# Kernel optimization log

Hardware: AMD Instinct MI355X
Metric: run time of the kernel (lower is better)

The kernel has to match this reference:

```python
import jax, jax.numpy as jnp
import numpy as np

ALPHA = 0.2  # LeakyReLU negative slope
NEG_INF = -9e15


def gat_layer(x, W, a, adj, concat):
    # x: [N, Fin], W: [Fin, Fout], a: [2*Fout, 1], adj: [N, N] (>0 = edge)
    h = x @ W                              # [N, Fout]
    Fout = W.shape[1]
    a_left = a[:Fout, 0]                   # scores from source (row) node
    a_right = a[Fout:, 0]                  # scores from target (col) node
    # e_ij = leakyrelu(a_left . h_i + a_right . h_j)  -- equivalent to the
    # concat-pairwise formulation without materializing [N, N, 2F]
    e = jax.nn.leaky_relu((h @ a_left)[:, None] + (h @ a_right)[None, :], ALPHA)
    e = jnp.where(adj > 0, e, NEG_INF)     # masked scores [N, N]
    att = jax.nn.softmax(e, axis=1)
    h_prime = att @ h                      # [N, Fout]
    return jax.nn.elu(h_prime) if concat else h_prime


def setup_inputs() -> dict:
    key = jax.random.key(0)
    ks = jax.random.split(key, 6)
    N, Din, Dh, Dout, H = 4096, 256, 64, 64, 8
    features = jax.random.normal(ks[0], (N, Din), dtype=jnp.float32)
    adj = jax.random.randint(ks[1], (N, N), 0, 2, dtype=jnp.int32)

    def xavier(k, shape, gain=1.414):
        fan_in, fan_out = shape[0], shape[1]
        bound = gain * np.sqrt(6.0 / (fan_in + fan_out))
        return jax.random.uniform(k, shape, jnp.float32, -bound, bound)

    W_h = jnp.stack([xavier(k, (Din, Dh)) for k in jax.random.split(ks[2], H)])        # [H, Din, Dh]
    a_h = jnp.stack([xavier(k, (2 * Dh, 1)) for k in jax.random.split(ks[3], H)])      # [H, 2Dh, 1]
    W_out = xavier(ks[4], (Dh * H, Dout))
    a_out = xavier(ks[5], (2 * Dout, 1))
    return {"features": features, "adj": adj, "W_h": W_h, "a_h": a_h,
            "W_out": W_out, "a_out": a_out}


def reference(features, adj, W_h, a_h, W_out, a_out):
    # eval mode: dropout layers are identity
    heads = jax.vmap(lambda W, a: gat_layer(features, W, a, adj, True))(W_h, a_h)  # [H, N, Dh]
    H, N, Dh = heads.shape
    x = jnp.transpose(heads, (1, 0, 2)).reshape(N, H * Dh)   # concat along feature dim
    return gat_layer(x, W_out, a_out, adj, False)            # [N, Dout]
```

## Files before the change

kernel.cpp:

```cpp
#include <hip/hip_runtime.h>
#include <hip/hip_fp16.h>

constexpr int NV  = 4096;
constexpr int DIN = 256;
constexpr int DH  = 64;
constexpr int NH  = 8;
constexpr int K2  = 512;
constexpr int Z2  = 8;

typedef _Float16 half8 __attribute__((ext_vector_type(8)));
typedef float f32x4 __attribute__((ext_vector_type(4)));
typedef unsigned u32x4 __attribute__((ext_vector_type(4)));

__device__ __forceinline__ unsigned fkey(float x) {
    unsigned b = __float_as_uint(x);
    return b ^ ((unsigned)((int)b >> 31) | 0x80000000u);
}
__device__ __forceinline__ float fkey_inv(unsigned key) {
    unsigned b = (key & 0x80000000u) ? (key ^ 0x80000000u) : ~key;
    return __uint_as_float(b);
}

__global__ void prep_kernel(const float* __restrict__ feat,
                            const float* __restrict__ Wh,
                            const float* __restrict__ ah,
                            const float* __restrict__ Wout,
                            const float* __restrict__ aout,
                            _Float16* __restrict__ xf16,
                            _Float16* __restrict__ WTh,
                            _Float16* __restrict__ WTo,
                            float* __restrict__ aLR,
                            unsigned* __restrict__ maxkey)
{
    int tid = blockIdx.x * blockDim.x + threadIdx.x;
    int nth = gridDim.x * blockDim.x;
    for (int i = tid; i < NV*DIN; i += nth) xf16[i] = (_Float16)feat[i];
    for (int i = tid; i < NH*DH*DIN; i += nth) {
        int h = i >> 14, n = (i >> 8) & 63, k = i & 255;
        WTh[i] = (_Float16)Wh[(h*DIN + k)*DH + n];
    }
    for (int i = tid; i < DH*K2; i += nth) {
        int n = i >> 9, k = i & 511;
        WTo[i] = (_Float16)Wout[k*DH + n];
    }
    for (int i = tid; i < NH*DH; i += nth) {
        int h = i >> 6, j = i & 63;
        aLR[i]          = ah[h*128 + j];
        aLR[NH*DH + i]  = ah[h*128 + 64 + j];
    }
    for (int i = tid; i < DH; i += nth) {
        aLR[2*NH*DH + i]      = aout[i];
        aLR[2*NH*DH + DH + i] = aout[64 + i];
    }
    if (tid < 16) maxkey[tid] = 0u;
}

__global__ void adjmask_kernel(const int* __restrict__ adj,
                               unsigned long long* __restrict__ mask)
{
    int row = blockIdx.x;
    int wave = threadIdx.x >> 6, lane = threadIdx.x & 63;
    for (int g = wave; g < 64; g += 4) {
        int v = adj[(size_t)row*NV + g*64 + lane];
        unsigned long long b = __ballot(v > 0);
        if (lane == 0) mask[(size_t)row*64 + g] = b;
    }
}

template<int K>
__global__ __launch_bounds__(256) void gemm_kernel(
    const _Float16* __restrict__ A,
    const _Float16* __restrict__ WT,
    const float* __restrict__ aL,
    const float* __restrict__ aR,
    _Float16* __restrict__ hT,
    float* __restrict__ hl,
    float* __restrict__ hr,
    unsigned* __restrict__ maxkey)
{
    const int head = blockIdx.y;
    const int i0 = blockIdx.x * 64;
    const int t = threadIdx.x;
    const int wave = t >> 6, lane = t & 63, m = lane & 15, q = lane >> 4;

    const _Float16* Ap = A + (size_t)(i0 + wave*16 + m) * K + q*8;
    const _Float16* Wp = WT + (size_t)head*DH*K + (size_t)m*K + q*8;

    f32x4 acc0 = {0.f,0.f,0.f,0.f}, acc1 = acc0, acc2 = acc0, acc3 = acc0;
    for (int k0 = 0; k0 < K; k0 += 32) {
        half8 a  = *(const half8*)(Ap + k0);
        half8 b0 = *(const half8*)(Wp + k0);
        half8 b1 = *(const half8*)(Wp + 16*K + k0);
        half8 b2 = *(const half8*)(Wp + 32*K + k0);
        half8 b3 = *(const half8*)(Wp + 48*K + k0);
        acc0 = __builtin_amdgcn_mfma_f32_16x16x32_f16(a, b0, acc0, 0, 0, 0);
        acc1 = __builtin_amdgcn_mfma_f32_16x16x32_f16(a, b1, acc1, 0, 0, 0);
        acc2 = __builtin_amdgcn_mfma_f32_16x16x32_f16(a, b2, acc2, 0, 0, 0);
        acc3 = __builtin_amdgcn_mfma_f32_16x16x32_f16(a, b3, acc3, 0, 0, 0);
    }

    __shared__ _Float16 T[64][80];
    const int rb = wave*16 + q*4;
    for (int r = 0; r < 4; r++) {
        T[ 0 + m][rb + r] = (_Float16)acc0[r];
        T[16 + m][rb + r] = (_Float16)acc1[r];
        T[32 + m][rb + r] = (_Float16)acc2[r];
        T[48 + m][rb + r] = (_Float16)acc3[r];
    }
    __syncthreads();

    {
        int d = t >> 2, seg = t & 3;
        half8* dst = (half8*)(hT + (size_t)(head*DH + d)*NV + i0 + seg*16);
        dst[0] = *(const half8*)&T[d][seg*16];
        dst[1] = *(const half8*)&T[d][seg*16 + 8];
    }
    __shared__ float red[2][4][64];
    {
        int il = t & 63, part = t >> 6;
        float sl = 0.f, sr = 0.f;
        for (int kk = 0; kk < 16; kk++) {
            int k = part*16 + kk;
            float hv = (float)T[k][il];
            sl += hv * aL[head*DH + k];
            sr += hv * aR[head*DH + k];
        }
        red[0][part][il] = sl;
        red[1][part][il] = sr;
    }
    __syncthreads();
    if (t < 64) {
        float sl = red[0][0][t] + red[0][1][t] + red[0][2][t] + red[0][3][t];
        float sr = red[1][0][t] + red[1][1][t] + red[1][2][t] + red[1][3][t];
        hl[head*NV + i0 + t] = sl;
        hr[head*NV + i0 + t] = sr;
        unsigned key = fkey(sr);
        for (int off = 32; off > 0; off >>= 1) {
            unsigned o = __shfl_xor(key, off);
            key = key > o ? key : o;
        }
        if (t == 0) atomicMax(maxkey + head, key);
    }
}

__global__ __launch_bounds__(256) void gemm2_kernel(
    const _Float16* __restrict__ A,
    const _Float16* __restrict__ WT,
    const float* __restrict__ aL,
    const float* __restrict__ aR,
    _Float16* __restrict__ hT,
    float* __restrict__ hl,
    float* __restrict__ hr,
    unsigned* __restrict__ maxkey)
{
    const int i0 = blockIdx.x * 16;
    const int t = threadIdx.x;
    const int w = t >> 6, lane = t & 63, m = lane & 15, q = lane >> 4;

    const _Float16* Ap = A + (size_t)(i0 + m)*K2 + w*128 + q*8;
    const _Float16* Wp = WT + (size_t)m*K2 + w*128 + q*8;

    f32x4 zero4 = {0.f,0.f,0.f,0.f};
    f32x4 acc[4] = {zero4, zero4, zero4, zero4};
    #pragma unroll
    for (int k0 = 0; k0 < 128; k0 += 32) {
        half8 a = *(const half8*)(Ap + k0);
        #pragma unroll
        for (int nt = 0; nt < 4; nt++) {
            half8 b = *(const half8*)(Wp + (size_t)nt*16*K2 + k0);
            acc[nt] = __builtin_amdgcn_mfma_f32_16x16x32_f16(a, b, acc[nt], 0, 0, 0);
        }
    }

    __shared__ float Cred[4][16][68];
    #pragma unroll
    for (int r = 0; r < 4; r++)
        #pragma unroll
        for (int nt = 0; nt < 4; nt++)
            Cred[w][q*4 + r][nt*16 + m] = acc[nt][r];
    __syncthreads();

    const int col = t & 63, r0 = (t >> 6) * 4;
    #pragma unroll
    for (int rr = 0; rr < 4; rr++) {
        int row = r0 + rr;
        float s = Cred[0][row][col] + Cred[1][row][col]
                + Cred[2][row][col] + Cred[3][row][col];
        hT[(size_t)col*NV + i0 + row] = (_Float16)s;
        Cred[0][row][col] = s;
    }
    __syncthreads();
    if (t < 16) {
        float sl = 0.f, sr = 0.f;
        for (int c = 0; c < 64; c++) {
            float v = Cred[0][t][c];
            sl += v * aL[c];
            sr += v * aR[c];
        }
        hl[i0 + t] = sl;
        hr[i0 + t] = sr;
        atomicMax(maxkey, fkey(sr));
    }
}

template<int MODE>
__global__ __launch_bounds__(256, 8) void att_kernel(
    const _Float16* __restrict__ hT,
    const float* __restrict__ hl,
    const float* __restrict__ hr,
    const unsigned* __restrict__ maxkey,
    const unsigned* __restrict__ adjm32,
    float* __restrict__ accz,
    float* __restrict__ lz)
{
    const int head = (MODE == 0) ? blockIdx.y : 0;
    const int i0 = blockIdx.x * 64;
    const int t = threadIdx.x;
    const int wave = t >> 6, lane = t & 63, m = lane & 15, q = lane >> 4;
    const int row = wave*16 + m;

    __shared__ _Float16 BT[64][136];
    __shared__ float hr1_s[128];
    __shared__ unsigned mask_s[64][4];
    __shared__ float a1_s[64], a2_s[64];

    const float L2E = 1.4426950408889634f;
    const float maxhr = fkey_inv(maxkey[head]);

    if (t < 64) {
        float v = hl[head*NV + i0 + t];
        float e = v + maxhr;
        float mi = fmaxf(e, 0.2f*e) * L2E;
        float a1 = v*L2E - mi;
        float a2 = 0.2f*L2E*v - mi;
        a1_s[t] = a1;
        a2_s[t] = a2 - 0.2f*a1;
    }

    f32x4 zero4 = {0.f,0.f,0.f,0.f};
    f32x4 acc[4] = {zero4, zero4, zero4, zero4};
    f32x4 accl = zero4;
    half8 ones;
    #pragma unroll
    for (int u = 0; u < 8; u++) ones[u] = (_Float16)1.0f;

    const int ntiles = 32 / gridDim.z;
    const int tile0  = blockIdx.z * ntiles;

    for (int tt = 0; tt < ntiles; tt++) {
        const int j0 = (tile0 + tt) * 128;
        #pragma unroll
        for (int ii = 0; ii < 4; ii++) {
            int d = (t >> 4) + ii*16;
            *(half8*)&BT[d][(t & 15)*8] =
                *(const half8*)(hT + (size_t)(head*DH + d)*NV + j0 + (t & 15)*8);
        }
        if (t < 128) hr1_s[t] = hr[head*NV + j0 + t] * L2E;
        mask_s[t >> 2][t & 3] = adjm32[(size_t)(i0 + (t >> 2))*128 + (j0 >> 5) + (t & 3)];
        __syncthreads();

        const float a1 = a1_s[row], a2p = a2_s[row];
        const u32x4 mkv = *(const u32x4*)&mask_s[row][0];
        #pragma unroll
        for (int ks = 0; ks < 4; ks++) {
            const int jj = ks*32 + q*8;
            const unsigned mk8 = mkv[ks] >> (q*8);
            f32x4 h0 = *(const f32x4*)&hr1_s[jj];
            f32x4 h1 = *(const f32x4*)&hr1_s[jj + 4];
            half8 a;
            #pragma unroll
            for (int u = 0; u < 8; u++) {
                float hv = (u < 4) ? h0[u] : h1[u - 4];
                float t1 = a1 + hv;
                float t2 = fmaf(0.2f, t1, a2p);
                float tm = fmaxf(t1, t2);
                tm = ((mk8 >> u) & 1u) ? tm : -10000.0f;
                a[u] = (_Float16)__builtin_amdgcn_exp2f(tm);
            }
            half8 b0 = *(const half8*)&BT[ 0 + m][jj];
            half8 b1 = *(const half8*)&BT[16 + m][jj];
            half8 b2 = *(const half8*)&BT[32 + m][jj];
            half8 b3 = *(const half8*)&BT[48 + m][jj];
            acc[0] = __builtin_amdgcn_mfma_f32_16x16x32_f16(a, b0, acc[0], 0, 0, 0);
            acc[1] = __builtin_amdgcn_mfma_f32_16x16x32_f16(a, b1, acc[1], 0, 0, 0);
            acc[2] = __builtin_amdgcn_mfma_f32_16x16x32_f16(a, b2, acc[2], 0, 0, 0);
            acc[3] = __builtin_amdgcn_mfma_f32_16x16x32_f16(a, b3, acc[3], 0, 0, 0);
            accl   = __builtin_amdgcn_mfma_f32_16x16x32_f16(a, ones, accl, 0, 0, 0);
        }
        __syncthreads();
    }

    #pragma unroll
    for (int r = 0; r < 4; r++) {
        const int orow = wave*16 + q*4 + r;
        const int i = i0 + orow;
        if (MODE == 0) {
            float* dst = accz + ((size_t)blockIdx.z*NV + i)*K2 + head*DH;
            #pragma unroll
            for (int nt = 0; nt < 4; nt++) dst[nt*16 + m] = acc[nt][r];
            if (m == 0) lz[((size_t)blockIdx.z*NH + head)*NV + i] = accl[r];
        } else {
            float* dst = accz + ((size_t)blockIdx.z*NV + i)*DH;
            #pragma unroll
            for (int nt = 0; nt < 4; nt++) dst[nt*16 + m] = acc[nt][r];
            if (m == 0) lz[(size_t)blockIdx.z*NV + i] = accl[r];
        }
    }
}

__global__ void combine_x2_kernel(const float* __restrict__ accz,
                                  const float* __restrict__ lz,
                                  _Float16* __restrict__ x2, int Z1)
{
    const float L2E = 1.4426950408889634f;
    int idx = blockIdx.x * blockDim.x + threadIdx.x;
    int i = idx >> 9, h = (idx & 511) >> 6;
    float s = 0.f, l = 0.f;
    for (int z = 0; z < Z1; z++) {
        s += accz[(size_t)z*NV*K2 + idx];
        l += lz[((size_t)z*NH + h)*NV + i];
    }
    float v = l > 0.f ? s / l : 0.f;
    v = v > 0.f ? v : (__builtin_amdgcn_exp2f(v * L2E) - 1.f);
    x2[idx] = (_Float16)v;
}

__global__ void finalize_kernel(const float* __restrict__ accz,
                                const float* __restrict__ lz,
                                float* __restrict__ out)
{
    int idx = blockIdx.x * blockDim.x + threadIdx.x;
    int i = idx >> 6;
    float s = 0.f, l = 0.f;
    #pragma unroll
    for (int z = 0; z < Z2; z++) {
        s += accz[(size_t)z*NV*DH + idx];
        l += lz[(size_t)z*NV + i];
    }
    out[idx] = l > 0.f ? s / l : 0.f;
}

extern "C" void kernel_launch(void* const* d_in, const int* in_sizes, int n_in,
                              void* d_out, int out_size, void* d_ws, size_t ws_size,
                              hipStream_t stream)
{
    const float* feat = (const float*)d_in[0];
    const int* adj    = (const int*)d_in[1];
    const float* Wh   = (const float*)d_in[2];
    const float* ah   = (const float*)d_in[3];
    const float* Wout = (const float*)d_in[4];
    const float* aout = (const float*)d_in[5];

    char* p = (char*)d_ws;
    auto alloc = [&](size_t bytes) { char* r = p; p += (bytes + 255) & ~255ull; return r; };

    _Float16* xf16 = (_Float16*)alloc((size_t)NV*DIN*2);
    _Float16* WTh  = (_Float16*)alloc((size_t)NH*DH*DIN*2);
    _Float16* WTo  = (_Float16*)alloc((size_t)DH*K2*2);
    float*    aLR  = (float*)alloc((2*NH*DH + 2*DH)*4);
    unsigned* maxkey = (unsigned*)alloc(16*4);
    unsigned long long* adjm = (unsigned long long*)alloc((size_t)NV*64*8);
    _Float16* hT1 = (_Float16*)alloc((size_t)NH*DH*NV*2);
    float* hl1 = (float*)alloc((size_t)NH*NV*4);
    float* hr1 = (float*)alloc((size_t)NH*NV*4);
    _Float16* x2  = (_Float16*)alloc((size_t)NV*K2*2);
    _Float16* hT2 = (_Float16*)alloc((size_t)DH*NV*2);
    float* acc2z = (float*)alloc((size_t)Z2*NV*DH*4);
    float* l2z   = (float*)alloc((size_t)Z2*NV*4);
    float* hl2 = (float*)alloc(NV*4);
    float* hr2 = (float*)alloc(NV*4);

    size_t used = (size_t)(p - (char*)d_ws);
    size_t per_z = (size_t)NV*K2*4 + (size_t)NH*NV*4 + 512;
    size_t avail = ws_size > used ? ws_size - used : 0;
    int Z1 = (avail >= 4*per_z + 4096) ? 4 : 2;
    float* acc1z = (float*)alloc((size_t)Z1*NV*K2*4);
    float* l1z   = (float*)alloc((size_t)Z1*NH*NV*4);

    prep_kernel<<<256, 256, 0, stream>>>(feat, Wh, ah, Wout, aout, xf16, WTh, WTo, aLR, maxkey);
    adjmask_kernel<<<NV, 256, 0, stream>>>(adj, adjm);
    gemm_kernel<DIN><<<dim3(64, NH), 256, 0, stream>>>(xf16, WTh, aLR, aLR + NH*DH,
                                                       hT1, hl1, hr1, maxkey);
    att_kernel<0><<<dim3(64, NH, Z1), 256, 0, stream>>>(hT1, hl1, hr1, maxkey,
                                                        (const unsigned*)adjm, acc1z, l1z);
    combine_x2_kernel<<<dim3(NV*K2/256), 256, 0, stream>>>(acc1z, l1z, x2, Z1);
    gemm2_kernel<<<dim3(NV/16), 256, 0, stream>>>(x2, WTo, aLR + 2*NH*DH, aLR + 2*NH*DH + DH,
                                                  hT2, hl2, hr2, maxkey + 8);
    att_kernel<1><<<dim3(64, 1, Z2), 256, 0, stream>>>(hT2, hl2, hr2, maxkey + 8,
                                                       (const unsigned*)adjm, acc2z, l2z);
    finalize_kernel<<<dim3(NV*DH/256), 256, 0, stream>>>(acc2z, l2z, (float*)d_out);
}
```

Baseline: 230.0 us.

## Factor attention exponentials into separable row/column terms and widen attention tiles

The per-element exp2 in the attention kernels is replaced by a factorization: exp(leakyrelu(l+r)) becomes the max of two products, exp(l)*exp(r) and exp(0.2l)*exp(0.2r). Each product is a precomputed fp16 row factor times a column factor, stabilised by a per-128-column tile max that the GEMM kernels now record with atomics. This removes per-element transcendental work, leaving a half-precision multiply, max and bitmask per element. Layer-one attention now processes two 16-row m-tiles per wave (128 rows per block) to reuse the loaded B tiles, with launch bounds relaxed to 4 blocks. The adjacency-bitmask kernel is merged into the prep kernel to save a launch. The risk is fp16 range and precision loss in the factored products. The kernel also now reads a single maxkey slot for every head, which only shifts a per-row constant.

```diff
diff --git a/kernel.cpp b/kernel.cpp
--- a/kernel.cpp
+++ b/kernel.cpp
@@ -21,7 +21,10 @@
     return __uint_as_float(b);
 }
 
+constexpr int NKEYS = 304;
+
 __global__ void prep_kernel(const float* __restrict__ feat,
+                            const int* __restrict__ adj,
                             const float* __restrict__ Wh,
                             const float* __restrict__ ah,
                             const float* __restrict__ Wout,
@@ -30,10 +33,21 @@
                             _Float16* __restrict__ WTh,
                             _Float16* __restrict__ WTo,
                             float* __restrict__ aLR,
-                            unsigned* __restrict__ maxkey)
-{
-    int tid = blockIdx.x * blockDim.x + threadIdx.x;
-    int nth = gridDim.x * blockDim.x;
+                            unsigned* __restrict__ keys,
+                            unsigned long long* __restrict__ mask)
+{
+    if (blockIdx.x < NV) {
+        int row = blockIdx.x;
+        int wave = threadIdx.x >> 6, lane = threadIdx.x & 63;
+        for (int g = wave; g < 64; g += 4) {
+            int v = adj[(size_t)row*NV + g*64 + lane];
+            unsigned long long b = __ballot(v > 0);
+            if (lane == 0) mask[(size_t)row*64 + g] = b;
+        }
+        return;
+    }
+    int tid = (blockIdx.x - NV) * blockDim.x + threadIdx.x;
+    int nth = 256 * 256;
     for (int i = tid; i < NV*DIN; i += nth) xf16[i] = (_Float16)feat[i];
     for (int i = tid; i < NH*DH*DIN; i += nth) {
         int h = i >> 14, n = (i >> 8) & 63, k = i & 255;
@@ -52,19 +66,7 @@
         aLR[2*NH*DH + i]      = aout[i];
         aLR[2*NH*DH + DH + i] = aout[64 + i];
     }
-    if (tid < 16) maxkey[tid] = 0u;
-}
-
-__global__ void adjmask_kernel(const int* __restrict__ adj,
-                               unsigned long long* __restrict__ mask)
-{
-    int row = blockIdx.x;
-    int wave = threadIdx.x >> 6, lane = threadIdx.x & 63;
-    for (int g = wave; g < 64; g += 4) {
-        int v = adj[(size_t)row*NV + g*64 + lane];
-        unsigned long long b = __ballot(v > 0);
-        if (lane == 0) mask[(size_t)row*64 + g] = b;
-    }
+    if (tid < NKEYS) keys[tid] = 0u;
 }
 
 template<int K>
@@ -76,7 +78,8 @@
     _Float16* __restrict__ hT,
     float* __restrict__ hl,
     float* __restrict__ hr,
-    unsigned* __restrict__ maxkey)
+    unsigned* __restrict__ maxkey,
+    unsigned* __restrict__ mtkey)
 {
     const int head = blockIdx.y;
     const int i0 = blockIdx.x * 64;
@@ -139,7 +142,10 @@
             unsigned o = __shfl_xor(key, off);
             key = key > o ? key : o;
         }
-        if (t == 0) atomicMax(maxkey + head, key);
+        if (t == 0) {
+            atomicMax(maxkey + head, key);
+            atomicMax(mtkey + head*32 + (i0 >> 7), key);
+        }
     }
 }
 
@@ -151,7 +157,8 @@
     _Float16* __restrict__ hT,
     float* __restrict__ hl,
     float* __restrict__ hr,
-    unsigned* __restrict__ maxkey)
+    unsigned* __restrict__ maxkey,
+    unsigned* __restrict__ mtkey)
 {
     const int i0 = blockIdx.x * 16;
     const int t = threadIdx.x;
@@ -199,47 +206,62 @@
         }
         hl[i0 + t] = sl;
         hr[i0 + t] = sr;
-        atomicMax(maxkey, fkey(sr));
-    }
-}
-
-template<int MODE>
-__global__ __launch_bounds__(256, 8) void att_kernel(
+        unsigned key = fkey(sr);
+        atomicMax(maxkey, key);
+        atomicMax(mtkey + (i0 >> 7), key);
+    }
+}
+
+template<int MODE, int NMT>
+__global__ __launch_bounds__(256, 4) void att_kernel(
     const _Float16* __restrict__ hT,
     const float* __restrict__ hl,
     const float* __restrict__ hr,
     const unsigned* __restrict__ maxkey,
+    const unsigned* __restrict__ mtkey,
     const unsigned* __restrict__ adjm32,
     float* __restrict__ accz,
     float* __restrict__ lz)
 {
     const int head = (MODE == 0) ? blockIdx.y : 0;
-    const int i0 = blockIdx.x * 64;
+    const int i0 = blockIdx.x * (NMT*64);
     const int t = threadIdx.x;
     const int wave = t >> 6, lane = t & 63, m = lane & 15, q = lane >> 4;
-    const int row = wave*16 + m;
 
     __shared__ _Float16 BT[64][136];
-    __shared__ float hr1_s[128];
-    __shared__ unsigned mask_s[64][4];
-    __shared__ float a1_s[64], a2_s[64];
+    __shared__ __align__(16) _Float16 Fs[128], Gs[128];
+    __shared__ __align__(16) unsigned mask_s[NMT*64][4];
+    __shared__ float b1_s[NMT*64], b2_s[NMT*64];
 
     const float L2E = 1.4426950408889634f;
-    const float maxhr = fkey_inv(maxkey[head]);
-
-    if (t < 64) {
+    const float maxhr = fkey_inv(*maxkey);
+
+    if (t < NMT*64) {
         float v = hl[head*NV + i0 + t];
-        float e = v + maxhr;
-        float mi = fmaxf(e, 0.2f*e) * L2E;
-        float a1 = v*L2E - mi;
-        float a2 = 0.2f*L2E*v - mi;
-        a1_s[t] = a1;
-        a2_s[t] = a2 - 0.2f*a1;
+        float X = v + maxhr;
+        float mm = fmaxf(X, 0.2f*X) * L2E;
+        b1_s[t] = __builtin_amdgcn_exp2f(v*L2E - mm);
+        b2_s[t] = __builtin_amdgcn_exp2f(0.2f*L2E*v - mm);
+    }
+    __syncthreads();
+
+    float b1r[NMT], b2r[NMT];
+    #pragma unroll
+    for (int mt = 0; mt < NMT; mt++) {
+        int row = wave*(NMT*16) + mt*16 + m;
+        b1r[mt] = b1_s[row];
+        b2r[mt] = b2_s[row];
     }
 
     f32x4 zero4 = {0.f,0.f,0.f,0.f};
-    f32x4 acc[4] = {zero4, zero4, zero4, zero4};
-    f32x4 accl = zero4;
+    f32x4 acc[NMT][4];
+    f32x4 accl[NMT];
+    #pragma unroll
+    for (int mt = 0; mt < NMT; mt++) {
+        accl[mt] = zero4;
+        #pragma unroll
+        for (int nt = 0; nt < 4; nt++) acc[mt][nt] = zero4;
+    }
     half8 ones;
     #pragma unroll
     for (int u = 0; u < 8; u++) ones[u] = (_Float16)1.0f;
@@ -255,55 +277,78 @@
             *(half8*)&BT[d][(t & 15)*8] =
                 *(const half8*)(hT + (size_t)(head*DH + d)*NV + j0 + (t & 15)*8);
         }
-        if (t < 128) hr1_s[t] = hr[head*NV + j0 + t] * L2E;
-        mask_s[t >> 2][t & 3] = adjm32[(size_t)(i0 + (t >> 2))*128 + (j0 >> 5) + (t & 3)];
+        const float mtv = fkey_inv(mtkey[(MODE == 0 ? head*32 : 0) + (j0 >> 7)]);
+        if (t < 128) {
+            float d = (hr[head*NV + j0 + t] - mtv) * L2E;
+            Fs[t] = (_Float16)__builtin_amdgcn_exp2f(d);
+            Gs[t] = (_Float16)__builtin_amdgcn_exp2f(0.2f*d);
+        }
+        if (t < NMT*64)
+            *(u32x4*)&mask_s[t][0] = *(const u32x4*)&adjm32[(size_t)(i0 + t)*128 + (j0 >> 5)];
         __syncthreads();
 
-        const float a1 = a1_s[row], a2p = a2_s[row];
-        const u32x4 mkv = *(const u32x4*)&mask_s[row][0];
+        const float s1 = __builtin_amdgcn_exp2f(mtv * L2E);
+        const float s2 = __builtin_amdgcn_exp2f(0.2f * mtv * L2E);
+        half8 e1v[NMT], e2v[NMT];
+        u32x4 mkv[NMT];
+        #pragma unroll
+        for (int mt = 0; mt < NMT; mt++) {
+            _Float16 e1 = (_Float16)(b1r[mt] * s1);
+            _Float16 e2 = (_Float16)(b2r[mt] * s2);
+            #pragma unroll
+            for (int u = 0; u < 8; u++) { e1v[mt][u] = e1; e2v[mt][u] = e2; }
+            mkv[mt] = *(const u32x4*)&mask_s[wave*(NMT*16) + mt*16 + m][0];
+        }
+
         #pragma unroll
         for (int ks = 0; ks < 4; ks++) {
             const int jj = ks*32 + q*8;
-            const unsigned mk8 = mkv[ks] >> (q*8);
-            f32x4 h0 = *(const f32x4*)&hr1_s[jj];
-            f32x4 h1 = *(const f32x4*)&hr1_s[jj + 4];
-            half8 a;
-            #pragma unroll
-            for (int u = 0; u < 8; u++) {
-                float hv = (u < 4) ? h0[u] : h1[u - 4];
-                float t1 = a1 + hv;
-                float t2 = fmaf(0.2f, t1, a2p);
-                float tm = fmaxf(t1, t2);
-                tm = ((mk8 >> u) & 1u) ? tm : -10000.0f;
-                a[u] = (_Float16)__builtin_amdgcn_exp2f(tm);
-            }
+            half8 F8 = *(const half8*)&Fs[jj];
+            half8 G8 = *(const half8*)&Gs[jj];
             half8 b0 = *(const half8*)&BT[ 0 + m][jj];
             half8 b1 = *(const half8*)&BT[16 + m][jj];
             half8 b2 = *(const half8*)&BT[32 + m][jj];
             half8 b3 = *(const half8*)&BT[48 + m][jj];
-            acc[0] = __builtin_amdgcn_mfma_f32_16x16x32_f16(a, b0, acc[0], 0, 0, 0);
-            acc[1] = __builtin_amdgcn_mfma_f32_16x16x32_f16(a, b1, acc[1], 0, 0, 0);
-            acc[2] = __builtin_amdgcn_mfma_f32_16x16x32_f16(a, b2, acc[2], 0, 0, 0);
-            acc[3] = __builtin_amdgcn_mfma_f32_16x16x32_f16(a, b3, acc[3], 0, 0, 0);
-            accl   = __builtin_amdgcn_mfma_f32_16x16x32_f16(a, ones, accl, 0, 0, 0);
+            #pragma unroll
+            for (int mt = 0; mt < NMT; mt++) {
+                const unsigned mk8 = (mkv[mt][ks] >> (q*8)) & 0xffu;
+                half8 t1 = e1v[mt] * F8;
+                half8 t2 = e2v[mt] * G8;
+                half8 am = __builtin_elementwise_max(t1, t2);
+                u32x4 av = __builtin_bit_cast(u32x4, am);
+                #pragma unroll
+                for (int pp = 0; pp < 4; pp++) {
+                    unsigned mw = ((0u - ((mk8 >> (2*pp)) & 1u)) & 0x0000FFFFu)
+                                | ((0u - ((mk8 >> (2*pp+1)) & 1u)) & 0xFFFF0000u);
+                    av[pp] &= mw;
+                }
+                half8 a = __builtin_bit_cast(half8, av);
+                acc[mt][0] = __builtin_amdgcn_mfma_f32_16x16x32_f16(a, b0, acc[mt][0], 0, 0, 0);
+                acc[mt][1] = __builtin_amdgcn_mfma_f32_16x16x32_f16(a, b1, acc[mt][1], 0, 0, 0);
+                acc[mt][2] = __builtin_amdgcn_mfma_f32_16x16x32_f16(a, b2, acc[mt][2], 0, 0, 0);
+                acc[mt][3] = __builtin_amdgcn_mfma_f32_16x16x32_f16(a, b3, acc[mt][3], 0, 0, 0);
+                accl[mt]   = __builtin_amdgcn_mfma_f32_16x16x32_f16(a, ones, accl[mt], 0, 0, 0);
+            }
         }
         __syncthreads();
     }
 
     #pragma unroll
-    for (int r = 0; r < 4; r++) {
-        const int orow = wave*16 + q*4 + r;
-        const int i = i0 + orow;
-        if (MODE == 0) {
-            float* dst = accz + ((size_t)blockIdx.z*NV + i)*K2 + head*DH;
-            #pragma unroll
-            for (int nt = 0; nt < 4; nt++) dst[nt*16 + m] = acc[nt][r];
-            if (m == 0) lz[((size_t)blockIdx.z*NH + head)*NV + i] = accl[r];
-        } else {
-            float* dst = accz + ((size_t)blockIdx.z*NV + i)*DH;
-            #pragma unroll
-            for (int nt = 0; nt < 4; nt++) dst[nt*16 + m] = acc[nt][r];
-            if (m == 0) lz[(size_t)blockIdx.z*NV + i] = accl[r];
+    for (int mt = 0; mt < NMT; mt++) {
+        #pragma unroll
+        for (int r = 0; r < 4; r++) {
+            const int i = i0 + wave*(NMT*16) + mt*16 + q*4 + r;
+            if (MODE == 0) {
+                float* dst = accz + ((size_t)blockIdx.z*NV + i)*K2 + head*DH;
+                #pragma unroll
+                for (int nt = 0; nt < 4; nt++) dst[nt*16 + m] = acc[mt][nt][r];
+                if (m == 0) lz[((size_t)blockIdx.z*NH + head)*NV + i] = accl[mt][r];
+            } else {
+                float* dst = accz + ((size_t)blockIdx.z*NV + i)*DH;
+                #pragma unroll
+                for (int nt = 0; nt < 4; nt++) dst[nt*16 + m] = acc[mt][nt][r];
+                if (m == 0) lz[(size_t)blockIdx.z*NV + i] = accl[mt][r];
+            }
         }
     }
 }
@@ -358,7 +403,7 @@
     _Float16* WTh  = (_Float16*)alloc((size_t)NH*DH*DIN*2);
     _Float16* WTo  = (_Float16*)alloc((size_t)DH*K2*2);
     float*    aLR  = (float*)alloc((2*NH*DH + 2*DH)*4);
-    unsigned* maxkey = (unsigned*)alloc(16*4);
+    unsigned* keys = (unsigned*)alloc(NKEYS*4);
     unsigned long long* adjm = (unsigned long long*)alloc((size_t)NV*64*8);
     _Float16* hT1 = (_Float16*)alloc((size_t)NH*DH*NV*2);
     float* hl1 = (float*)alloc((size_t)NH*NV*4);
@@ -377,16 +422,20 @@
     float* acc1z = (float*)alloc((size_t)Z1*NV*K2*4);
     float* l1z   = (float*)alloc((size_t)Z1*NH*NV*4);
 
-    prep_kernel<<<256, 256, 0, stream>>>(feat, Wh, ah, Wout, aout, xf16, WTh, WTo, aLR, maxkey);
-    adjmask_kernel<<<NV, 256, 0, stream>>>(adj, adjm);
+    unsigned* maxkey = keys;
+    unsigned* mtk1   = keys + 16;
+    unsigned* mtk2   = keys + 272;
+
+    prep_kernel<<<NV + 256, 256, 0, stream>>>(feat, adj, Wh, ah, Wout, aout,
+                                              xf16, WTh, WTo, aLR, keys, adjm);
     gemm_kernel<DIN><<<dim3(64, NH), 256, 0, stream>>>(xf16, WTh, aLR, aLR + NH*DH,
-                                                       hT1, hl1, hr1, maxkey);
-    att_kernel<0><<<dim3(64, NH, Z1), 256, 0, stream>>>(hT1, hl1, hr1, maxkey,
-                                                        (const unsigned*)adjm, acc1z, l1z);
+                                                       hT1, hl1, hr1, maxkey, mtk1);
+    att_kernel<0, 2><<<dim3(NV/128, NH, Z1), 256, 0, stream>>>(
+        hT1, hl1, hr1, maxkey, mtk1, (const unsigned*)adjm, acc1z, l1z);
     combine_x2_kernel<<<dim3(NV*K2/256), 256, 0, stream>>>(acc1z, l1z, x2, Z1);
     gemm2_kernel<<<dim3(NV/16), 256, 0, stream>>>(x2, WTo, aLR + 2*NH*DH, aLR + 2*NH*DH + DH,
-                                                  hT2, hl2, hr2, maxkey + 8);
-    att_kernel<1><<<dim3(64, 1, Z2), 256, 0, stream>>>(hT2, hl2, hr2, maxkey + 8,
-                                                       (const unsigned*)adjm, acc2z, l2z);
+                                                  hT2, hl2, hr2, maxkey + 8, mtk2);
+    att_kernel<1, 1><<<dim3(NV/64, 1, Z2), 256, 0, stream>>>(
+        hT2, hl2, hr2, maxkey + 8, mtk2, (const unsigned*)adjm, acc2z, l2z);
     finalize_kernel<<<dim3(NV*DH/256), 256, 0, stream>>>(acc2z, l2z, (float*)d_out);
 }
```

Result: faster. 199.3 us (median of 2 runs) (-13.4%).
